# Kernel tuning notes

Measured on AMD Instinct MI355X. Metric: run time of the kernel, lower is better.

The kernel has to match this reference:

```python
import jax, jax.numpy as jnp
import numpy as np

BSZ, SEQ, D_IN = 256, 512, 1
STATE, D_OUT, KX = 512, 512, 5


def setup_inputs() -> dict:
    key = jax.random.key(0)
    k1, k2, k3, k4, k5, k6 = jax.random.split(key, 6)
    inputs = jax.random.normal(k1, (BSZ, SEQ, D_IN), dtype=jnp.float32)
    # diagonal transition, kept stable in (0, 0.99)
    A = jax.random.uniform(k2, (STATE,), dtype=jnp.float32, minval=0.0, maxval=0.99)
    B = jax.random.normal(k3, (D_IN, STATE), dtype=jnp.float32) * 0.05
    C = jax.random.normal(k4, (STATE, D_OUT), dtype=jnp.float32) * 0.05
    M = jax.random.normal(k5, (D_OUT, D_IN, KX), dtype=jnp.float32) * 0.05
    h0 = jax.random.normal(k6, (STATE,), dtype=jnp.float32)
    return {"inputs": inputs, "A": A, "B": B, "C": C, "M": M, "h0": h0}


def reference(inputs, A, B, C, M, h0):
    """LDS forward: h_t = A*h_{t-1} + x_t @ B; y_t = h_t @ C + sum_i M[:,:,i] x_{t-1-i}.
    inputs: [B, T, 1] -> out: [B, T, D_OUT]
    """
    bsz, T, _ = inputs.shape
    h_init = jnp.broadcast_to(h0, (bsz, h0.shape[0]))  # reset_state: h = h0 per batch row

    xs = jnp.swapaxes(inputs, 0, 1)  # [T, B, 1]

    def step(h, x_t):
        h = h * A + x_t @ B  # [B, STATE]
        return h, h

    _, hs = jax.lax.scan(step, h_init, xs)  # hs: [T, B, STATE]
    lds_out = jnp.einsum('tbs,so->bto', hs, C)  # [B, T, D_OUT]

    # AR ring buffer: at step t it holds x_{t-1}..x_{t-kx} (zeros before t=0),
    # tap i multiplies M[:,:,i]. With d_in==1 this is a delayed causal conv.
    x = inputs[:, :, 0]  # [B, T]
    kx = M.shape[-1]
    shifted = jnp.stack(
        [jnp.pad(x, ((0, 0), (i + 1, 0)))[:, :T] for i in range(kx)], axis=-1
    )  # [B, T, kx]; entry i is x_{t-1-i}
    ar_out = jnp.einsum('btk,ok->bto', shifted, M[:, 0, :])  # [B, T, D_OUT]

    return lds_out + ar_out
```

## Files before the change

### kernel.cpp

```cpp
#include <hip/hip_runtime.h>


typedef __attribute__((ext_vector_type(8))) short short8v;
typedef __attribute__((ext_vector_type(4))) float float4v;

#define NB 16
#define SIG(e) ((e) + ((e) >> 3))

static __device__ __forceinline__ unsigned short f2bf(float f) {
    union { float f; unsigned int u; } x; x.f = f;
    unsigned int r = x.u + 0x7fffu + ((x.u >> 16) & 1u);
    return (unsigned short)(r >> 16);
}

__global__ __launch_bounds__(256) void k_prep(const float* __restrict__ A,
                                              const float* __restrict__ B,
                                              const float* __restrict__ h0,
                                              const float* __restrict__ C,
                                              const float* __restrict__ M,
                                              const float* __restrict__ x,
                                              unsigned short* __restrict__ KT,
                                              float* __restrict__ G,
                                              short8v* __restrict__ XS) {
    __shared__ float PBL[512][4];
    __shared__ float PHL[512][4];
    __shared__ float red[4][64][8];
    __shared__ unsigned short xs[512];
    const int tid = threadIdx.x;

    if (blockIdx.x < 1024) {
        const int d0 = (blockIdx.x & 127) * 4;
        const int oc = blockIdx.x >> 7;

        #pragma unroll
        for (int q = 0; q < 2; ++q) {
            int ss = tid + q * 256;
            float a = A[ss];
            float r = 1.0f, base = a;
            #pragma unroll
            for (int bit = 0; bit < 9; ++bit) {
                if (d0 & (1 << bit)) r *= base;
                base *= base;
            }
            float bs = B[ss], hs = h0[ss];
            #pragma unroll
            for (int j = 0; j < 4; ++j) {
                PBL[ss][j] = r * bs;
                PHL[ss][j] = r * a * hs;
                r *= a;
            }
        }
        __syncthreads();

        const int lane = tid & 63;
        const int sc   = tid >> 6;
        const int o    = oc * 64 + lane;
        float kt[4] = {0.f, 0.f, 0.f, 0.f};
        float gg[4] = {0.f, 0.f, 0.f, 0.f};
        #pragma unroll 4
        for (int si = 0; si < 128; ++si) {
            int s = sc * 128 + si;
            float c = C[s * 512 + o];
            #pragma unroll
            for (int j = 0; j < 4; ++j) {
                kt[j] = fmaf(PBL[s][j], c, kt[j]);
                gg[j] = fmaf(PHL[s][j], c, gg[j]);
            }
        }
        #pragma unroll
        for (int j = 0; j < 4; ++j) {
            red[sc][lane][j]     = kt[j];
            red[sc][lane][j + 4] = gg[j];
        }
        __syncthreads();
        if (sc == 0) {
            #pragma unroll
            for (int j = 0; j < 4; ++j) {
                float v  = red[0][lane][j] + red[1][lane][j]
                         + red[2][lane][j] + red[3][lane][j];
                float gv = red[0][lane][j+4] + red[1][lane][j+4]
                         + red[2][lane][j+4] + red[3][lane][j+4];
                int d = d0 + j;
                if (d >= 1 && d <= 5) v += M[o * 5 + (d - 1)];
                KT[o * 512 + d] = f2bf(v);
                G[d * 512 + o]  = gv;
            }
        }
    } else {
        const int b = blockIdx.x - 1024;
        #pragma unroll
        for (int q = 0; q < 2; ++q) {
            int i = tid * 2 + q;
            xs[i] = f2bf(x[b * 512 + 511 - i]);
        }
        __syncthreads();
        short8v* dst = XS + (size_t)b * 1216;
        for (int s2 = tid; s2 < 1216; s2 += 256) {
            if (s2 % 9 == 8 || s2 > 1150) dst[s2] = (short8v)(short)0;
        }
        #pragma unroll
        for (int q = 0; q < 4; ++q) {
            int e = tid * 4 + q;
            short8v v;
            #pragma unroll
            for (int jj = 0; jj < 8; ++jj) {
                int i = e + jj;
                v[jj] = (i < 512) ? (short)xs[i] : (short)0;
            }
            dst[SIG(e)] = v;
        }
    }
}

__global__ __launch_bounds__(512, 2) void k_main(const short8v* __restrict__ XS,
                                                 const unsigned short* __restrict__ KT,
                                                 const float* __restrict__ G,
                                                 float* __restrict__ out) {
    __shared__ short8v xbuf[2][1216];

    const int bo0 = blockIdx.x * 32;
    const int b0  = blockIdx.y * NB;
    const int tid = threadIdx.x;
    const int lane = tid & 63;
    const int w    = tid >> 6;
    const int wm   = w >> 1, wn = w & 1;
    const int t0w  = wm * 128;
    const int lrow = lane & 15;
    const int g    = lane >> 4;
    const int o0w  = bo0 + wn * 16;
    const int ocol = o0w + g * 4;

    const short8v* s0 = XS + (size_t)b0 * 1216;
    short8v x0 = s0[tid], x1 = s0[tid + 512], x2;
    if (tid < 192) x2 = s0[tid + 1024];

    short8v bfr[16];
    {
        const unsigned short* bp = KT + (o0w + lrow) * 512 + g * 8;
        #pragma unroll
        for (int ks = 0; ks < 16; ++ks)
            bfr[ks] = *(const short8v*)(bp + ks * 32);
    }

    float4v gacc[8];
    #pragma unroll
    for (int mi = 0; mi < 8; ++mi)
        gacc[mi] = *(const float4v*)(G + (t0w + mi * 16 + lrow) * 512 + ocol);

    xbuf[0][tid] = x0;
    xbuf[0][tid + 512] = x1;
    if (tid < 192) xbuf[0][tid + 1024] = x2;
    __syncthreads();

    const int E0 = 511 - t0w - lrow + g * 8;

    int p = 0;
    for (int bi = 0; bi < NB; ++bi) {
        const int b = b0 + bi;

        short8v nx0, nx1, nx2;
        if (bi + 1 < NB) {
            const short8v* s = XS + (size_t)(b + 1) * 1216;
            nx0 = s[tid];
            nx1 = s[tid + 512];
            if (tid < 192) nx2 = s[tid + 1024];
        }

        const short8v* xo = xbuf[p];

        float4v acc[8];
        #pragma unroll
        for (int mi = 0; mi < 8; ++mi) acc[mi] = (float4v)(0.0f);

        short8v aw[8];
        #pragma unroll
        for (int j = -7; j <= 0; ++j)
            aw[j & 7] = xo[SIG(E0 + 16 * j)];

        #pragma unroll
        for (int ks = 0; ks < 16; ++ks) {
            acc[7] = __builtin_amdgcn_mfma_f32_16x16x32_bf16(
                bfr[ks], aw[(2 * ks - 7) & 7], acc[7], 0, 0, 0);
            acc[6] = __builtin_amdgcn_mfma_f32_16x16x32_bf16(
                bfr[ks], aw[(2 * ks - 6) & 7], acc[6], 0, 0, 0);
            if (ks < 15) {
                aw[(2 * ks + 1) & 7] = xo[SIG(E0 + 16 * (2 * ks + 1))];
                aw[(2 * ks + 2) & 7] = xo[SIG(E0 + 16 * (2 * ks + 2))];
            }
            #pragma unroll
            for (int mi = 5; mi >= 0; --mi)
                acc[mi] = __builtin_amdgcn_mfma_f32_16x16x32_bf16(
                    bfr[ks], aw[(2 * ks - mi) & 7], acc[mi], 0, 0, 0);
        }

        float* op = out + (size_t)b * 262144;
        #pragma unroll
        for (int mi = 0; mi < 8; ++mi) {
            const int t = t0w + mi * 16 + lrow;
            *(float4v*)(op + t * 512 + ocol) = acc[mi] + gacc[mi];
        }

        if (bi + 1 < NB) {
            short8v* xw = xbuf[p ^ 1];
            xw[tid] = nx0;
            xw[tid + 512] = nx1;
            if (tid < 192) xw[tid + 1024] = nx2;
            asm volatile("s_waitcnt lgkmcnt(0)" ::: "memory");
            __builtin_amdgcn_s_barrier();
            p ^= 1;
        }
    }
}

extern "C" void kernel_launch(void* const* d_in, const int* in_sizes, int n_in,
                              void* d_out, int out_size, void* d_ws, size_t ws_size,
                              hipStream_t stream) {
    const float* x  = (const float*)d_in[0];
    const float* A  = (const float*)d_in[1];
    const float* B  = (const float*)d_in[2];
    const float* C  = (const float*)d_in[3];
    const float* M  = (const float*)d_in[4];
    const float* h0 = (const float*)d_in[5];
    float* out = (float*)d_out;

    char* ws = (char*)d_ws;
    unsigned short* KT = (unsigned short*)ws;
    float*          G  = (float*)(ws + (1u << 19));
    short8v*        XS = (short8v*)(ws + (1u << 19) + (1u << 20));

    k_prep<<<1280, 256, 0, stream>>>(A, B, h0, C, M, x, KT, G, XS);
    k_main<<<dim3(16, 16), 512, 0, stream>>>(XS, KT, G, out);
}
```

Measured before the change: 85.52 us.

## Retile main kernel waves to 64x32 and use direct global-to-LDS async loads

Each wave in the main kernel now covers 64 time rows across both 16-wide output column blocks, instead of 128 rows by 16 columns. Every shifted input fragment read from LDS therefore feeds two MFMAs, which cuts LDS read traffic and shrinks the sliding window from 8 to 6 registers, at the cost of holding twice as many B fragments in registers. The next batch's input is prefetched with global_load_lds straight into the LDS double buffer, removing the register staging and the explicit LDS stores. The wait is a vmcnt(8) that depends on the outstanding output stores being counted. The prep kernel also batches eight C loads per iteration to expose more memory-level parallelism.

```diff
diff --git a/kernel.cpp b/kernel.cpp
--- a/kernel.cpp
+++ b/kernel.cpp
@@ -6,6 +6,7 @@
 
 #define NB 16
 #define SIG(e) ((e) + ((e) >> 3))
+#define AWI(j) ((((j) % 6) + 6) % 6)
 
 static __device__ __forceinline__ unsigned short f2bf(float f) {
     union { float f; unsigned int u; } x; x.f = f;
@@ -57,14 +58,19 @@
         const int o    = oc * 64 + lane;
         float kt[4] = {0.f, 0.f, 0.f, 0.f};
         float gg[4] = {0.f, 0.f, 0.f, 0.f};
-        #pragma unroll 4
-        for (int si = 0; si < 128; ++si) {
-            int s = sc * 128 + si;
-            float c = C[s * 512 + o];
-            #pragma unroll
-            for (int j = 0; j < 4; ++j) {
-                kt[j] = fmaf(PBL[s][j], c, kt[j]);
-                gg[j] = fmaf(PHL[s][j], c, gg[j]);
+        for (int si = 0; si < 128; si += 8) {
+            float c8[8];
+            #pragma unroll
+            for (int u = 0; u < 8; ++u)
+                c8[u] = C[(sc * 128 + si + u) * 512 + o];
+            #pragma unroll
+            for (int u = 0; u < 8; ++u) {
+                int s = sc * 128 + si + u;
+                #pragma unroll
+                for (int j = 0; j < 4; ++j) {
+                    kt[j] = fmaf(PBL[s][j], c8[u], kt[j]);
+                    gg[j] = fmaf(PHL[s][j], c8[u], gg[j]);
+                }
             }
         }
         #pragma unroll
@@ -122,35 +128,39 @@
     const int b0  = blockIdx.y * NB;
     const int tid = threadIdx.x;
     const int lane = tid & 63;
-    const int w    = tid >> 6;
-    const int wm   = w >> 1, wn = w & 1;
-    const int t0w  = wm * 128;
+    const int wv   = tid >> 6;
+    const int t0w  = wv * 64;
     const int lrow = lane & 15;
     const int g    = lane >> 4;
-    const int o0w  = bo0 + wn * 16;
-    const int ocol = o0w + g * 4;
-
-    const short8v* s0 = XS + (size_t)b0 * 1216;
-    short8v x0 = s0[tid], x1 = s0[tid + 512], x2;
-    if (tid < 192) x2 = s0[tid + 1024];
-
-    short8v bfr[16];
+
     {
-        const unsigned short* bp = KT + (o0w + lrow) * 512 + g * 8;
+        const short8v* src = XS + (size_t)b0 * 1216;
+        for (int c = wv; c < 19; c += 8)
+            __builtin_amdgcn_global_load_lds(
+                (const __attribute__((address_space(1))) void*)(src + c * 64 + lane),
+                (__attribute__((address_space(3))) void*)(&xbuf[0][c * 64]),
+                16, 0, 0);
+    }
+
+    short8v bfr[2][16];
+    #pragma unroll
+    for (int ni = 0; ni < 2; ++ni) {
+        const unsigned short* bp = KT + (bo0 + ni * 16 + lrow) * 512 + g * 8;
         #pragma unroll
         for (int ks = 0; ks < 16; ++ks)
-            bfr[ks] = *(const short8v*)(bp + ks * 32);
-    }
-
-    float4v gacc[8];
+            bfr[ni][ks] = *(const short8v*)(bp + ks * 32);
+    }
+
+    float4v gacc[4][2];
     #pragma unroll
-    for (int mi = 0; mi < 8; ++mi)
-        gacc[mi] = *(const float4v*)(G + (t0w + mi * 16 + lrow) * 512 + ocol);
-
-    xbuf[0][tid] = x0;
-    xbuf[0][tid + 512] = x1;
-    if (tid < 192) xbuf[0][tid + 1024] = x2;
-    __syncthreads();
+    for (int mi = 0; mi < 4; ++mi)
+        #pragma unroll
+        for (int ni = 0; ni < 2; ++ni)
+            gacc[mi][ni] = *(const float4v*)(G + (t0w + mi * 16 + lrow) * 512
+                                               + bo0 + ni * 16 + g * 4);
+
+    asm volatile("s_waitcnt vmcnt(0)" ::: "memory");
+    __builtin_amdgcn_s_barrier();
 
     const int E0 = 511 - t0w - lrow + g * 8;
 
@@ -158,54 +168,65 @@
     for (int bi = 0; bi < NB; ++bi) {
         const int b = b0 + bi;
 
-        short8v nx0, nx1, nx2;
         if (bi + 1 < NB) {
-            const short8v* s = XS + (size_t)(b + 1) * 1216;
-            nx0 = s[tid];
-            nx1 = s[tid + 512];
-            if (tid < 192) nx2 = s[tid + 1024];
+            const short8v* src = XS + (size_t)(b + 1) * 1216;
+            short8v* dstb = xbuf[p ^ 1];
+            for (int c = wv; c < 19; c += 8)
+                __builtin_amdgcn_global_load_lds(
+                    (const __attribute__((address_space(1))) void*)(src + c * 64 + lane),
+                    (__attribute__((address_space(3))) void*)(dstb + c * 64),
+                    16, 0, 0);
         }
 
         const short8v* xo = xbuf[p];
 
-        float4v acc[8];
-        #pragma unroll
-        for (int mi = 0; mi < 8; ++mi) acc[mi] = (float4v)(0.0f);
-
-        short8v aw[8];
-        #pragma unroll
-        for (int j = -7; j <= 0; ++j)
-            aw[j & 7] = xo[SIG(E0 + 16 * j)];
+        float4v acc[4][2];
+        #pragma unroll
+        for (int mi = 0; mi < 4; ++mi)
+            #pragma unroll
+            for (int ni = 0; ni < 2; ++ni)
+                acc[mi][ni] = (float4v)(0.0f);
+
+        short8v aw[6];
+        #pragma unroll
+        for (int j = -3; j <= 0; ++j)
+            aw[AWI(j)] = xo[SIG(E0 + 16 * j)];
 
         #pragma unroll
         for (int ks = 0; ks < 16; ++ks) {
-            acc[7] = __builtin_amdgcn_mfma_f32_16x16x32_bf16(
-                bfr[ks], aw[(2 * ks - 7) & 7], acc[7], 0, 0, 0);
-            acc[6] = __builtin_amdgcn_mfma_f32_16x16x32_bf16(
-                bfr[ks], aw[(2 * ks - 6) & 7], acc[6], 0, 0, 0);
+            acc[3][0] = __builtin_amdgcn_mfma_f32_16x16x32_bf16(
+                bfr[0][ks], aw[AWI(2 * ks - 3)], acc[3][0], 0, 0, 0);
+            acc[3][1] = __builtin_amdgcn_mfma_f32_16x16x32_bf16(
+                bfr[1][ks], aw[AWI(2 * ks - 3)], acc[3][1], 0, 0, 0);
+            acc[2][0] = __builtin_amdgcn_mfma_f32_16x16x32_bf16(
+                bfr[0][ks], aw[AWI(2 * ks - 2)], acc[2][0], 0, 0, 0);
+            acc[2][1] = __builtin_amdgcn_mfma_f32_16x16x32_bf16(
+                bfr[1][ks], aw[AWI(2 * ks - 2)], acc[2][1], 0, 0, 0);
             if (ks < 15) {
-                aw[(2 * ks + 1) & 7] = xo[SIG(E0 + 16 * (2 * ks + 1))];
-                aw[(2 * ks + 2) & 7] = xo[SIG(E0 + 16 * (2 * ks + 2))];
-            }
-            #pragma unroll
-            for (int mi = 5; mi >= 0; --mi)
-                acc[mi] = __builtin_amdgcn_mfma_f32_16x16x32_bf16(
-                    bfr[ks], aw[(2 * ks - mi) & 7], acc[mi], 0, 0, 0);
+                aw[AWI(2 * ks + 1)] = xo[SIG(E0 + 16 * (2 * ks + 1))];
+                aw[AWI(2 * ks + 2)] = xo[SIG(E0 + 16 * (2 * ks + 2))];
+            }
+            acc[1][0] = __builtin_amdgcn_mfma_f32_16x16x32_bf16(
+                bfr[0][ks], aw[AWI(2 * ks - 1)], acc[1][0], 0, 0, 0);
+            acc[1][1] = __builtin_amdgcn_mfma_f32_16x16x32_bf16(
+                bfr[1][ks], aw[AWI(2 * ks - 1)], acc[1][1], 0, 0, 0);
+            acc[0][0] = __builtin_amdgcn_mfma_f32_16x16x32_bf16(
+                bfr[0][ks], aw[AWI(2 * ks)], acc[0][0], 0, 0, 0);
+            acc[0][1] = __builtin_amdgcn_mfma_f32_16x16x32_bf16(
+                bfr[1][ks], aw[AWI(2 * ks)], acc[0][1], 0, 0, 0);
         }
 
         float* op = out + (size_t)b * 262144;
         #pragma unroll
-        for (int mi = 0; mi < 8; ++mi) {
+        for (int mi = 0; mi < 4; ++mi) {
             const int t = t0w + mi * 16 + lrow;
-            *(float4v*)(op + t * 512 + ocol) = acc[mi] + gacc[mi];
+            float* rp = op + t * 512 + bo0 + g * 4;
+            *(float4v*)(rp)      = acc[mi][0] + gacc[mi][0];
+            *(float4v*)(rp + 16) = acc[mi][1] + gacc[mi][1];
         }
 
         if (bi + 1 < NB) {
-            short8v* xw = xbuf[p ^ 1];
-            xw[tid] = nx0;
-            xw[tid + 512] = nx1;
-            if (tid < 192) xw[tid + 1024] = nx2;
-            asm volatile("s_waitcnt lgkmcnt(0)" ::: "memory");
+            asm volatile("s_waitcnt vmcnt(8)" ::: "memory");
             __builtin_amdgcn_s_barrier();
             p ^= 1;
         }
```

Result: slower. 91.70 us (+7.2%).
